# Kernel optimization log

Measured on AMD Instinct MI355X. Metric: run time of the kernel, lower is better.

Reference implementation:

```python
import jax, jax.numpy as jnp
import numpy as np

B, T, HIDDEN = 1, 2048, 2048
N_HEADS, N_KV_HEADS, HEAD_DIM = 32, 8, 64
N_KV_GROUPS = N_HEADS // N_KV_HEADS
MAX_POS = 8192


def _rope_tables(seq_len, head_dim, dtype):
    inv_freq = 1.0 / (10000.0 ** (jnp.arange(0, head_dim, 2, dtype=jnp.float32) / head_dim))
    t = jnp.arange(seq_len, dtype=jnp.float32)
    freqs = jnp.einsum('i,j->ij', t, inv_freq)          # [T, head_dim//2]
    emb = jnp.concatenate([freqs, freqs], axis=-1)      # [T, head_dim]
    cos = jnp.cos(emb)[None, None].astype(dtype)        # [1,1,T,head_dim]
    sin = jnp.sin(emb)[None, None].astype(dtype)
    return cos, sin


def _apply_rotary(x, cos, sin):
    # faithful to original: interleaved rotate-half with cat(freqs,freqs) tables
    x1, x2 = x[..., ::2], x[..., 1::2]
    x_rot = jnp.stack([-x2, x1], axis=-1).reshape(x.shape)
    return x * cos + x_rot * sin


def setup_inputs() -> dict:
    key = jax.random.key(0)
    kx, kq, kk, kv, ko = jax.random.split(key, 5)
    s = 0.02
    return {
        'x':  jax.random.normal(kx, (B, T, HIDDEN), dtype=jnp.float32),
        'Wq': s * jax.random.normal(kq, (N_HEADS * HEAD_DIM, HIDDEN), dtype=jnp.float32),
        'Wk': s * jax.random.normal(kk, (N_KV_HEADS * HEAD_DIM, HIDDEN), dtype=jnp.float32),
        'Wv': s * jax.random.normal(kv, (N_KV_HEADS * HEAD_DIM, HIDDEN), dtype=jnp.float32),
        'Wo': s * jax.random.normal(ko, (HIDDEN, HIDDEN), dtype=jnp.float32),
    }


def reference(x, Wq, Wk, Wv, Wo):
    Bv, Tv, _ = x.shape
    dtype = x.dtype
    # projections (torch Linear: y = x @ W.T), reshape to [B, heads, T, head_dim]
    q = jnp.einsum('bth,oh->bto', x, Wq).reshape(Bv, Tv, N_HEADS, HEAD_DIM).transpose(0, 2, 1, 3)
    k = jnp.einsum('bth,oh->bto', x, Wk).reshape(Bv, Tv, N_KV_HEADS, HEAD_DIM).transpose(0, 2, 1, 3)
    v = jnp.einsum('bth,oh->bto', x, Wv).reshape(Bv, Tv, N_KV_HEADS, HEAD_DIM).transpose(0, 2, 1, 3)
    cos, sin = _rope_tables(Tv, HEAD_DIM, dtype)
    q = _apply_rotary(q, cos, sin)
    k = _apply_rotary(k, cos, sin)
    if N_KV_GROUPS != 1:
        k = jnp.repeat(k, N_KV_GROUPS, axis=1)   # [B, n_heads, T, d]
        v = jnp.repeat(v, N_KV_GROUPS, axis=1)
    scale = 1.0 / jnp.sqrt(jnp.asarray(HEAD_DIM, dtype=dtype))
    scores = jnp.einsum('bhtd,bhsd->bhts', q, k) * scale   # [B,H,T,T]
    causal = jnp.tril(jnp.ones((Tv, Tv), dtype=bool))
    scores = jnp.where(causal[None, None], scores, jnp.asarray(-jnp.inf, dtype=dtype))
    attn = jax.nn.softmax(scores, axis=-1)
    out = jnp.einsum('bhts,bhsd->bhtd', attn, v)
    out = out.transpose(0, 2, 1, 3).reshape(Bv, Tv, HIDDEN)
    return jnp.einsum('bth,oh->bto', out, Wo)
```

## Files before the change

### kernel.cpp

```cpp
#include <hip/hip_runtime.h>
#include <hip/hip_bf16.h>
#include <stdint.h>

#define TT 2048
#define HID 2048
#define NH 32
#define NKV 8
#define HD 64

typedef __attribute__((ext_vector_type(4))) float f32x4;
typedef __attribute__((ext_vector_type(16))) float f32x16;
typedef __attribute__((ext_vector_type(8))) short bf16x8;

__device__ __forceinline__ unsigned short f2bf(float f) {
  unsigned int u = __builtin_bit_cast(unsigned int, f);
  unsigned int r = (u + 0x7FFFu + ((u >> 16) & 1u)) >> 16;
  return (unsigned short)r;
}
__device__ __forceinline__ float bf2f(unsigned short h) {
  unsigned int u = ((unsigned int)h) << 16;
  return __builtin_bit_cast(float, u);
}
__device__ __forceinline__ unsigned int cvtpk(float lo, float hi) {
  unsigned int d;
  asm("v_cvt_pk_bf16_f32 %0, %1, %2" : "=v"(d) : "v"(lo), "v"(hi));
  return d;
}
__device__ __forceinline__ float max3f(float a, float b, float c) {
  float d;
  asm("v_max3_f32 %0, %1, %2, %3" : "=v"(d) : "v"(a), "v"(b), "v"(c));
  return d;
}

__device__ __forceinline__ void gld_lds16(const void* g, void* l) {
  __builtin_amdgcn_global_load_lds(
      (const __attribute__((address_space(1))) unsigned int*)g,
      (__attribute__((address_space(3))) unsigned int*)l,
      16, 0, 0);
}

__global__ __launch_bounds__(256)
void k_cvt_all(const float* __restrict__ x, const float* __restrict__ wq,
               const float* __restrict__ wk, const float* __restrict__ wv,
               const float* __restrict__ wo,
               unsigned short* __restrict__ xb, unsigned short* __restrict__ wqb,
               unsigned short* __restrict__ wkb, unsigned short* __restrict__ wvb,
               unsigned short* __restrict__ wob) {
  int i = blockIdx.x * 256 + threadIdx.x;
  const float* src; unsigned short* dst; int off;
  if      (i < 1048576) { src = x;  dst = xb;  off = i; }
  else if (i < 2097152) { src = wq; dst = wqb; off = i - 1048576; }
  else if (i < 2359296) { src = wk; dst = wkb; off = i - 2097152; }
  else if (i < 2621440) { src = wv; dst = wvb; off = i - 2359296; }
  else if (i < 3670016) { src = wo; dst = wob; off = i - 2621440; }
  else return;
  const float4 v = reinterpret_cast<const float4*>(src)[off];
  ushort4 o;
  o.x = f2bf(v.x); o.y = f2bf(v.y); o.z = f2bf(v.z); o.w = f2bf(v.w);
  reinterpret_cast<ushort4*>(dst)[off] = o;
}

__device__ __forceinline__ void stage_tile(const unsigned short* __restrict__ g,
                                           unsigned short* lds, int w, int l, int k0) {
#pragma unroll
  for (int j = 0; j < 2; ++j) {
    const int cbase = w * 128 + j * 64;
    const int c = cbase + l;
    const int row = c >> 2, off = c & 3;
    gld_lds16(g + row * 2048 + k0 + off * 8, lds + cbase * 8);
  }
}

__device__ __forceinline__ void gemm_core(const unsigned short* __restrict__ A,
                                          const unsigned short* __restrict__ B,
                                          unsigned short* As, unsigned short* Bs,
                                          f32x4 (&acc)[4][4], int kiters) {
  const int tid = threadIdx.x;
  const int l = tid & 63, w = tid >> 6;
  const int wm = w >> 1, wn = w & 1;
  const int ll = l & 15, lg = l >> 4;

  stage_tile(A, As, w, l, 0);
  stage_tile(B, Bs, w, l, 0);
  int cur = 0;
  for (int kt = 0; kt < kiters; ++kt) {
    __syncthreads();
    if (kt + 1 < kiters) {
      stage_tile(A, As + (cur ^ 1) * 4096, w, l, (kt + 1) * 32);
      stage_tile(B, Bs + (cur ^ 1) * 4096, w, l, (kt + 1) * 32);
    }
    const unsigned short* a0 = As + cur * 4096;
    const unsigned short* b0 = Bs + cur * 4096;
    bf16x8 af[4], bfr[4];
#pragma unroll
    for (int i = 0; i < 4; ++i) {
      af[i]  = *reinterpret_cast<const bf16x8*>(a0 + (wm * 64 + i * 16 + ll) * 32 + lg * 8);
      bfr[i] = *reinterpret_cast<const bf16x8*>(b0 + (wn * 64 + i * 16 + ll) * 32 + lg * 8);
    }
#pragma unroll
    for (int i = 0; i < 4; ++i)
#pragma unroll
      for (int j = 0; j < 4; ++j)
        acc[i][j] = __builtin_amdgcn_mfma_f32_16x16x32_bf16(af[i], bfr[j], acc[i][j], 0, 0, 0);
    cur ^= 1;
  }
}

__global__ __launch_bounds__(256)
void k_gemm_qkv(const unsigned short* __restrict__ xb,
                const unsigned short* __restrict__ wq,
                const unsigned short* __restrict__ wk,
                const unsigned short* __restrict__ wv,
                unsigned short* __restrict__ Pq,
                unsigned short* __restrict__ Pk,
                unsigned short* __restrict__ Pv) {
  __shared__ __align__(16) unsigned short As[2 * 4096];
  __shared__ __align__(16) unsigned short Bs[2 * 4096];
  const int bid = blockIdx.x;
  const unsigned short *A, *B;
  int m0, n0, seg, ks;
  if (bid < 640) {
    ks = bid & 1;
    int pair = bid >> 1;
    int mt = pair / 20, nt = pair % 20;
    m0 = mt * 128;
    A = xb + (size_t)m0 * 2048 + ks * 1024;
    if (nt < 16) { seg = 0; n0 = nt * 128; B = wq + (size_t)n0 * 2048 + ks * 1024; }
    else         { seg = 1; n0 = (nt - 16) * 128; B = wk + (size_t)n0 * 2048 + ks * 1024; }
  } else {
    int vb = bid - 640;
    ks = vb & 1;
    int pair = vb >> 1;
    int mt = pair / 16, nt = pair % 16;
    seg = 2; m0 = mt * 128; n0 = nt * 128;
    A = wv + (size_t)m0 * 2048 + ks * 1024;
    B = xb + (size_t)n0 * 2048 + ks * 1024;
  }
  f32x4 acc[4][4] = {};
  gemm_core(A, B, As, Bs, acc, 32);

  const int l = threadIdx.x & 63, w = threadIdx.x >> 6;
  const int wm = w >> 1, wn = w & 1;
#pragma unroll
  for (int i = 0; i < 4; ++i)
#pragma unroll
    for (int j = 0; j < 4; ++j)
#pragma unroll
      for (int r = 0; r < 4; ++r) {
        int row = m0 + wm * 64 + i * 16 + ((l >> 4) << 2) + r;
        int col = n0 + wn * 64 + j * 16 + (l & 15);
        unsigned short v = f2bf(acc[i][j][r]);
        if (seg == 0)      Pq[(size_t)ks * 4194304 + (size_t)row * 2048 + col] = v;
        else if (seg == 1) Pk[(size_t)ks * 1048576 + (size_t)row * 512 + col] = v;
        else               Pv[(size_t)ks * 1048576 + (size_t)row * 2048 + col] = v;
      }
}

__global__ __launch_bounds__(256)
void k_gemm_out(const unsigned short* __restrict__ Ob,
                const unsigned short* __restrict__ wo,
                float* __restrict__ out,
                float* __restrict__ p1a, float* __restrict__ p1b) {
  __shared__ __align__(16) unsigned short As[2 * 4096];
  __shared__ __align__(16) unsigned short Bs[2 * 4096];
  const int bid = blockIdx.x;
  const int ks = bid >> 8;
  const int rem = bid & 255;
  const int m0 = (rem >> 4) * 128, n0 = (rem & 15) * 128;
  f32x4 acc[4][4] = {};
  gemm_core(Ob + (size_t)m0 * 2048 + ks * 1024,
            wo + (size_t)n0 * 2048 + ks * 1024, As, Bs, acc, 32);

  const int l = threadIdx.x & 63, w = threadIdx.x >> 6;
  const int wm = w >> 1, wn = w & 1;
#pragma unroll
  for (int i = 0; i < 4; ++i)
#pragma unroll
    for (int j = 0; j < 4; ++j)
#pragma unroll
      for (int r = 0; r < 4; ++r) {
        int row = m0 + wm * 64 + i * 16 + ((l >> 4) << 2) + r;
        int col = n0 + wn * 64 + j * 16 + (l & 15);
        if (ks == 0) {
          out[(size_t)row * HID + col] = acc[i][j][r];
        } else {
          float* p = (row < 1024) ? (p1a + (size_t)row * HID)
                                  : (p1b + (size_t)(row - 1024) * HID);
          p[col] = acc[i][j][r];
        }
      }
}

__global__ __launch_bounds__(256)
void k_reduce_out(float* __restrict__ out,
                  const float* __restrict__ p1a, const float* __restrict__ p1b) {
  const int i = blockIdx.x * 256 + threadIdx.x;
  const int row = i >> 9;
  const float* p1 = (row < 1024) ? p1a : (p1b - (size_t)1024 * HID);
  const float4 a = reinterpret_cast<const float4*>(out)[i];
  const float4 b = reinterpret_cast<const float4*>(p1)[i];
  float4 c;
  c.x = a.x + b.x; c.y = a.y + b.y; c.z = a.z + b.z; c.w = a.w + b.w;
  reinterpret_cast<float4*>(out)[i] = c;
}

__global__ __launch_bounds__(256)
void k_rope_tab(float2* __restrict__ tab) {
  const int i = blockIdx.x * 256 + threadIdx.x;
  const int t = i >> 6, k = i & 63;
  const float cexp = -13.287712379549449f / 32.0f;
  const float fr = exp2f((float)(k & 31) * cexp);
  const float a = (float)t * fr;
  tab[i] = make_float2(__cosf(a), __sinf(a));
}

__global__ __launch_bounds__(256)
void k_rope_kv(const unsigned short* __restrict__ Pk,
               const unsigned short* __restrict__ Pv,
               const float2* __restrict__ tab,
               unsigned short* __restrict__ Kb,
               unsigned short* __restrict__ VT) {
  int p = blockIdx.x * 256 + threadIdx.x;
  if (p < 524288) {
    const int t = p >> 8;
    const int col2 = (p & 255) * 2;
    const int kh = col2 >> 6, d = col2 & 63;
    const unsigned int u0 = *reinterpret_cast<const unsigned int*>(Pk + (size_t)t * 512 + col2);
    const unsigned int u1 = *reinterpret_cast<const unsigned int*>(Pk + 1048576 + (size_t)t * 512 + col2);
    float x0 = bf2f((unsigned short)(u0 & 0xFFFFu)) + bf2f((unsigned short)(u1 & 0xFFFFu));
    float x1 = bf2f((unsigned short)(u0 >> 16)) + bf2f((unsigned short)(u1 >> 16));
    const float4 cs = *reinterpret_cast<const float4*>(tab + t * 64 + d);
    float o0 = x0 * cs.x - x1 * cs.y;
    float o1 = x1 * cs.z + x0 * cs.w;
    unsigned int pw = (unsigned int)f2bf(o0) | ((unsigned int)f2bf(o1) << 16);
    *reinterpret_cast<unsigned int*>(Kb + ((size_t)kh * 2048 + t) * 64 + d) = pw;
  } else {
    const int i2 = (p - 524288) * 2;
    const unsigned int u0 = *reinterpret_cast<const unsigned int*>(Pv + i2);
    const unsigned int u1 = *reinterpret_cast<const unsigned int*>(Pv + 1048576 + i2);
    float x0 = bf2f((unsigned short)(u0 & 0xFFFFu)) + bf2f((unsigned short)(u1 & 0xFFFFu));
    float x1 = bf2f((unsigned short)(u0 >> 16)) + bf2f((unsigned short)(u1 >> 16));
    unsigned int pw = (unsigned int)f2bf(x0) | ((unsigned int)f2bf(x1) << 16);
    *reinterpret_cast<unsigned int*>(VT + i2) = pw;
  }
}

__global__ __launch_bounds__(256)
void k_rope_q(const unsigned short* __restrict__ Pq,
              const float2* __restrict__ tab,
              unsigned short* __restrict__ Qb) {
  const int p = blockIdx.x * 256 + threadIdx.x;
  const int t = p >> 10;
  const int col2 = (p & 1023) * 2;
  const int h = col2 >> 6, d = col2 & 63;
  const unsigned int u0 = *reinterpret_cast<const unsigned int*>(Pq + (size_t)t * 2048 + col2);
  const unsigned int u1 = *reinterpret_cast<const unsigned int*>(Pq + 4194304 + (size_t)t * 2048 + col2);
  float x0 = bf2f((unsigned short)(u0 & 0xFFFFu)) + bf2f((unsigned short)(u1 & 0xFFFFu));
  float x1 = bf2f((unsigned short)(u0 >> 16)) + bf2f((unsigned short)(u1 >> 16));
  const float scale = 0.125f * 1.4426950408889634f;
  const float4 cs = *reinterpret_cast<const float4*>(tab + t * 64 + d);
  float o0 = (x0 * cs.x - x1 * cs.y) * scale;
  float o1 = (x1 * cs.z + x0 * cs.w) * scale;
  unsigned int pw = (unsigned int)f2bf(o0) | ((unsigned int)f2bf(o1) << 16);
  *reinterpret_cast<unsigned int*>(Qb + ((size_t)h * 2048 + t) * 64 + d) = pw;
}

__device__ __forceinline__ void attn_stage(const unsigned short* __restrict__ Kg,
                                           const unsigned short* __restrict__ Vg,
                                           unsigned short* Ks, unsigned short* Vs,
                                           int kv0, int w, int l) {
#pragma unroll
  for (int j = 0; j < 4; ++j) {
    const int cb = j * 128 + w * 64;
    const int c = cb + l;
    const int row = c >> 3;
    const int src8 = ((c & 7) ^ (row & 7)) * 8;
    gld_lds16(Kg + (size_t)(kv0 + row) * 64 + src8, Ks + cb * 8);
    gld_lds16(Vg + (size_t)row * TT + kv0 + src8, Vs + cb * 8);
  }
}

__global__ __launch_bounds__(128, 2)
void k_attn(const unsigned short* __restrict__ Qb,
            const unsigned short* __restrict__ Kb,
            const unsigned short* __restrict__ VT,
            unsigned short* __restrict__ Ob) {
  __shared__ __align__(16) unsigned short Ks[2][64 * 64];
  __shared__ __align__(16) unsigned short Vs[2][64 * 64];
  const int b = blockIdx.x;
  const int h = b & 31;
  const int qi = b >> 5;
  const int q0 = qi & 7, kq = qi >> 3;
  const int qt = (kq == 0) ? 2 * q0 : (kq == 1) ? 31 - 2 * q0
               : (kq == 2) ? 2 * q0 + 1 : 30 - 2 * q0;
  const int kh = h >> 2;
  const int tid = threadIdx.x;
  const int l = tid & 63, w = tid >> 6;
  const int q = l & 31, hi = l >> 5;
  const int qrow = qt * 64 + w * 32 + q;

  const unsigned short* Qh = Qb + (size_t)h * TT * 64;
  const unsigned short* Kh = Kb + (size_t)kh * TT * 64;
  const unsigned short* Vh = VT + (size_t)kh * 64 * TT;

  bf16x8 qf[4];
#pragma unroll
  for (int s = 0; s < 4; ++s)
    qf[s] = *reinterpret_cast<const bf16x8*>(Qh + (size_t)qrow * 64 + s * 16 + hi * 8);

  f32x16 ot0, ot1;
#pragma unroll
  for (int r = 0; r < 16; ++r) { ot0[r] = 0.f; ot1[r] = 0.f; }
  float m = -3e38f, lsum = 0.f;
  const int nkt = qt + 1;

  attn_stage(Kh, Vh, Ks[0], Vs[0], 0, w, l);
  int cur = 0;
  for (int kt = 0; kt < nkt; ++kt) {
    __syncthreads();
    if (kt + 1 < nkt)
      attn_stage(Kh, Vh, Ks[cur ^ 1], Vs[cur ^ 1], (kt + 1) * 64, w, l);

    const char* Kc = reinterpret_cast<const char*>(Ks[cur]);
    const char* Vc = reinterpret_cast<const char*>(Vs[cur]);

    f32x16 s0, s1;
#pragma unroll
    for (int r = 0; r < 16; ++r) { s0[r] = 0.f; s1[r] = 0.f; }
    __builtin_amdgcn_s_setprio(1);
#pragma unroll
    for (int s = 0; s < 4; ++s) {
      const int chunk = 2 * s + hi;
      const bf16x8 kf0 = *reinterpret_cast<const bf16x8*>(
          Kc + q * 128 + ((chunk ^ (q & 7)) * 16));
      const bf16x8 kf1 = *reinterpret_cast<const bf16x8*>(
          Kc + (32 + q) * 128 + ((chunk ^ (q & 7)) * 16));
      s0 = __builtin_amdgcn_mfma_f32_32x32x16_bf16(kf0, qf[s], s0, 0, 0, 0);
      s1 = __builtin_amdgcn_mfma_f32_32x32x16_bf16(kf1, qf[s], s1, 0, 0, 0);
    }
    __builtin_amdgcn_s_setprio(0);
    if (kt == qt) {
#pragma unroll
      for (int r = 0; r < 16; ++r) {
        const int kvr = kt * 64 + (r & 3) + 8 * (r >> 2) + 4 * hi;
        if (kvr > qrow) s0[r] = -3e38f;
        if (kvr + 32 > qrow) s1[r] = -3e38f;
      }
    }
    float a0 = max3f(s0[0], s0[1], s0[2]);
    float a1 = max3f(s0[3], s0[4], s0[5]);
    float a2 = max3f(s0[6], s0[7], s0[8]);
    float a3 = max3f(s0[9], s0[10], s0[11]);
    float a4 = max3f(s0[12], s0[13], s0[14]);
    float a5 = max3f(s0[15], s1[0], s1[1]);
    float a6 = max3f(s1[2], s1[3], s1[4]);
    float a7 = max3f(s1[5], s1[6], s1[7]);
    float a8 = max3f(s1[8], s1[9], s1[10]);
    float a9 = max3f(s1[11], s1[12], s1[13]);
    float a10 = fmaxf(s1[14], s1[15]);
    float b0 = max3f(a0, a1, a2);
    float b1 = max3f(a3, a4, a5);
    float b2 = max3f(a6, a7, a8);
    float b3 = fmaxf(a9, a10);
    float mloc = fmaxf(max3f(b0, b1, b2), b3);
    mloc = fmaxf(mloc, __shfl_xor(mloc, 32));

    if (!__all(mloc <= m + 8.f)) {
      const float mn = fmaxf(m, mloc);
      const float al = __builtin_amdgcn_exp2f(m - mn);
      m = mn;
      lsum *= al;
#pragma unroll
      for (int r = 0; r < 16; ++r) { ot0[r] *= al; ot1[r] *= al; }
    }
#pragma unroll
    for (int r = 0; r < 16; ++r) {
      s0[r] = __builtin_amdgcn_exp2f(s0[r] - m);
      s1[r] = __builtin_amdgcn_exp2f(s1[r] - m);
    }
    float t16[16];
#pragma unroll
    for (int r = 0; r < 16; ++r) t16[r] = s0[r] + s1[r];
#pragma unroll
    for (int r = 0; r < 8; ++r) t16[r] += t16[r + 8];
#pragma unroll
    for (int r = 0; r < 4; ++r) t16[r] += t16[r + 4];
    float ssum = (t16[0] + t16[1]) + (t16[2] + t16[3]);
    ssum += __shfl_xor(ssum, 32);
    lsum += ssum;

#pragma unroll
    for (int s = 0; s < 4; ++s) {
      const int base = (s & 1) * 8;
      const f32x16& sg = (s < 2) ? s0 : s1;
      const unsigned int c0 = cvtpk(sg[base + 0], sg[base + 1]);
      const unsigned int c1 = cvtpk(sg[base + 2], sg[base + 3]);
      const unsigned int c2 = cvtpk(sg[base + 4], sg[base + 5]);
      const unsigned int c3 = cvtpk(sg[base + 6], sg[base + 7]);
      const unsigned int slo = hi ? c0 : c2, shi_ = hi ? c1 : c3;
      const unsigned int rlo = (unsigned int)__shfl_xor((int)slo, 32);
      const unsigned int rhi = (unsigned int)__shfl_xor((int)shi_, 32);
      union { unsigned int u[4]; bf16x8 v; } P;
      P.u[0] = hi ? rlo : c0;
      P.u[1] = hi ? rhi : c1;
      P.u[2] = hi ? c2 : rlo;
      P.u[3] = hi ? c3 : rhi;
      const int chunk = 2 * s + hi;
      const bf16x8 vf0 = *reinterpret_cast<const bf16x8*>(
          Vc + q * 128 + ((chunk ^ (q & 7)) * 16));
      const bf16x8 vf1 = *reinterpret_cast<const bf16x8*>(
          Vc + (32 + q) * 128 + ((chunk ^ (q & 7)) * 16));
      __builtin_amdgcn_s_setprio(1);
      ot0 = __builtin_amdgcn_mfma_f32_32x32x16_bf16(vf0, P.v, ot0, 0, 0, 0);
      ot1 = __builtin_amdgcn_mfma_f32_32x32x16_bf16(vf1, P.v, ot1, 0, 0, 0);
      __builtin_amdgcn_s_setprio(0);
    }
    cur ^= 1;
  }

  __syncthreads();
  float* Of = reinterpret_cast<float*>(&Ks[0][0]) + w * (64 * 33);
  const float inv = 1.0f / lsum;
#pragma unroll
  for (int r = 0; r < 16; ++r) {
    const int d = (r & 3) + 8 * (r >> 2) + 4 * hi;
    Of[d * 33 + q] = ot0[r] * inv;
    Of[(d + 32) * 33 + q] = ot1[r] * inv;
  }
  __syncthreads();
#pragma unroll
  for (int i = 0; i < 4; ++i) {
    const int a = 4 * hi + i;
    float v[8];
#pragma unroll
    for (int k2 = 0; k2 < 8; ++k2) v[k2] = Of[(a * 8 + k2) * 33 + q];
    union { unsigned int u[4]; uint4 vec; } O4;
    O4.u[0] = cvtpk(v[0], v[1]);
    O4.u[1] = cvtpk(v[2], v[3]);
    O4.u[2] = cvtpk(v[4], v[5]);
    O4.u[3] = cvtpk(v[6], v[7]);
    *reinterpret_cast<uint4*>(Ob + (size_t)qrow * HID + h * 64 + a * 8) = O4.vec;
  }
}

extern "C" void kernel_launch(void* const* d_in, const int* in_sizes, int n_in,
                              void* d_out, int out_size, void* d_ws, size_t ws_size,
                              hipStream_t stream) {
  const float* x  = (const float*)d_in[0];
  const float* Wq = (const float*)d_in[1];
  const float* Wk = (const float*)d_in[2];
  const float* Wv = (const float*)d_in[3];
  const float* Wo = (const float*)d_in[4];
  float* out = (float*)d_out;
  char* ws = (char*)d_ws;

  unsigned short* xb  = (unsigned short*)(ws);
  unsigned short* wqb = (unsigned short*)(ws + (8u  << 20));
  unsigned short* wkb = (unsigned short*)(ws + (16u << 20));
  unsigned short* wvb = (unsigned short*)(ws + (18u << 20));
  unsigned short* wob = (unsigned short*)(ws + (20u << 20));
  unsigned short* Qb  = (unsigned short*)(ws + (28u << 20));
  unsigned short* Kb  = (unsigned short*)(ws + (36u << 20));
  unsigned short* VT  = (unsigned short*)(ws + (38u << 20));
  unsigned short* Ob  = xb;
  float2* tab = (float2*)(ws + (8u << 20));
  unsigned short* Pq = (unsigned short*)d_out;
  unsigned short* Pk = (unsigned short*)(ws + (28u << 20));
  unsigned short* Pv = (unsigned short*)(ws + (32u << 20));
  float* p1a = (float*)(ws + (8u << 20));
  float* p1b = (float*)(ws + (28u << 20));

  k_cvt_all<<<14336, 256, 0, stream>>>(x, Wq, Wk, Wv, Wo, xb, wqb, wkb, wvb, wob);
  k_gemm_qkv<<<768, 256, 0, stream>>>(xb, wqb, wkb, wvb, Pq, Pk, Pv);
  k_rope_tab<<<512, 256, 0, stream>>>(tab);
  k_rope_kv<<<4096, 256, 0, stream>>>(Pk, Pv, tab, Kb, VT);
  k_rope_q<<<8192, 256, 0, stream>>>(Pq, tab, Qb);
  k_attn<<<dim3(1024), 128, 0, stream>>>(Qb, Kb, VT, Ob);
  k_gemm_out<<<512, 256, 0, stream>>>(Ob, wob, out, p1a, p1b);
  k_reduce_out<<<4096, 256, 0, stream>>>(out, p1a, p1b);
}
```

Baseline: 163.3 us.

## Split long causal query tiles across two blocks and merge partial softmax results

```diff
diff --git a/kernel.cpp b/kernel.cpp
--- a/kernel.cpp
+++ b/kernel.cpp
@@ -271,12 +271,11 @@
                                            int kv0, int w, int l) {
 #pragma unroll
   for (int j = 0; j < 4; ++j) {
-    const int cb = j * 128 + w * 64;
-    const int c = cb + l;
-    const int row = c >> 3;
-    const int src8 = ((c & 7) ^ (row & 7)) * 8;
-    gld_lds16(Kg + (size_t)(kv0 + row) * 64 + src8, Ks + cb * 8);
-    gld_lds16(Vg + (size_t)row * TT + kv0 + src8, Vs + cb * 8);
+    const int c = j * 2 + w;
+    unsigned short* kd = Ks + c * 512;
+    unsigned short* vd = Vs + c * 512;
+    gld_lds16(Kg + (size_t)(kv0 + l) * 64 + c * 8, kd);
+    gld_lds16(Vg + (size_t)l * TT + kv0 + c * 8, vd);
   }
 }
 
@@ -284,15 +283,20 @@
 void k_attn(const unsigned short* __restrict__ Qb,
             const unsigned short* __restrict__ Kb,
             const unsigned short* __restrict__ VT,
-            unsigned short* __restrict__ Ob) {
+            unsigned short* __restrict__ Ob,
+            float* __restrict__ PA, float* __restrict__ PB,
+            float* __restrict__ MLb) {
   __shared__ __align__(16) unsigned short Ks[2][64 * 64];
   __shared__ __align__(16) unsigned short Vs[2][64 * 64];
   const int b = blockIdx.x;
   const int h = b & 31;
-  const int qi = b >> 5;
-  const int q0 = qi & 7, kq = qi >> 3;
-  const int qt = (kq == 0) ? 2 * q0 : (kq == 1) ? 31 - 2 * q0
-               : (kq == 2) ? 2 * q0 + 1 : 30 - 2 * q0;
+  const int u = b >> 5;
+  int qt, kt0, kt1, mode;
+  if (u < 16)      { qt = 16 + u; kt0 = 0;  kt1 = 15; mode = 1; }
+  else if (u < 24) { qt = 47 - u; kt0 = 16; kt1 = qt; mode = 2; }
+  else if (u < 32) { qt = u - 8;  kt0 = 16; kt1 = qt; mode = 2; }
+  else if (u < 40) { qt = 47 - u; kt0 = 0;  kt1 = qt; mode = 0; }
+  else             { qt = u - 40; kt0 = 0;  kt1 = qt; mode = 0; }
   const int kh = h >> 2;
   const int tid = threadIdx.x;
   const int l = tid & 63, w = tid >> 6;
@@ -312,17 +316,16 @@
 #pragma unroll
   for (int r = 0; r < 16; ++r) { ot0[r] = 0.f; ot1[r] = 0.f; }
   float m = -3e38f, lsum = 0.f;
-  const int nkt = qt + 1;
-
-  attn_stage(Kh, Vh, Ks[0], Vs[0], 0, w, l);
+
+  attn_stage(Kh, Vh, Ks[0], Vs[0], kt0 * 64, w, l);
   int cur = 0;
-  for (int kt = 0; kt < nkt; ++kt) {
+  for (int kt = kt0; kt <= kt1; ++kt) {
     __syncthreads();
-    if (kt + 1 < nkt)
+    if (kt + 1 <= kt1)
       attn_stage(Kh, Vh, Ks[cur ^ 1], Vs[cur ^ 1], (kt + 1) * 64, w, l);
 
-    const char* Kc = reinterpret_cast<const char*>(Ks[cur]);
-    const char* Vc = reinterpret_cast<const char*>(Vs[cur]);
+    const unsigned short* Kc = Ks[cur];
+    const unsigned short* Vc = Vs[cur];
 
     f32x16 s0, s1;
 #pragma unroll
@@ -330,11 +333,9 @@
     __builtin_amdgcn_s_setprio(1);
 #pragma unroll
     for (int s = 0; s < 4; ++s) {
-      const int chunk = 2 * s + hi;
-      const bf16x8 kf0 = *reinterpret_cast<const bf16x8*>(
-          Kc + q * 128 + ((chunk ^ (q & 7)) * 16));
-      const bf16x8 kf1 = *reinterpret_cast<const bf16x8*>(
-          Kc + (32 + q) * 128 + ((chunk ^ (q & 7)) * 16));
+      const int c = 2 * s + hi;
+      const bf16x8 kf0 = *reinterpret_cast<const bf16x8*>(Kc + (c * 64 + q) * 8);
+      const bf16x8 kf1 = *reinterpret_cast<const bf16x8*>(Kc + (c * 64 + 32 + q) * 8);
       s0 = __builtin_amdgcn_mfma_f32_32x32x16_bf16(kf0, qf[s], s0, 0, 0, 0);
       s1 = __builtin_amdgcn_mfma_f32_32x32x16_bf16(kf1, qf[s], s1, 0, 0, 0);
     }
@@ -405,11 +406,9 @@
       P.u[1] = hi ? rhi : c1;
       P.u[2] = hi ? c2 : rlo;
       P.u[3] = hi ? c3 : rhi;
-      const int chunk = 2 * s + hi;
-      const bf16x8 vf0 = *reinterpret_cast<const bf16x8*>(
-          Vc + q * 128 + ((chunk ^ (q & 7)) * 16));
-      const bf16x8 vf1 = *reinterpret_cast<const bf16x8*>(
-          Vc + (32 + q) * 128 + ((chunk ^ (q & 7)) * 16));
+      const int c = 2 * s + hi;
+      const bf16x8 vf0 = *reinterpret_cast<const bf16x8*>(Vc + (c * 64 + q) * 8);
+      const bf16x8 vf1 = *reinterpret_cast<const bf16x8*>(Vc + (c * 64 + 32 + q) * 8);
       __builtin_amdgcn_s_setprio(1);
       ot0 = __builtin_amdgcn_mfma_f32_32x32x16_bf16(vf0, P.v, ot0, 0, 0, 0);
       ot1 = __builtin_amdgcn_mfma_f32_32x32x16_bf16(vf1, P.v, ot1, 0, 0, 0);
@@ -418,6 +417,20 @@
     cur ^= 1;
   }
 
+  if (mode) {
+    const int pid = (qt - 16) * 32 + h;
+    float* P = (mode == 1 ? PA : PB) + (size_t)pid * 4096 + w * 2048;
+#pragma unroll
+    for (int r = 0; r < 16; ++r) {
+      P[r * 64 + l] = ot0[r];
+      P[(16 + r) * 64 + l] = ot1[r];
+    }
+    const int mlidx = (mode == 1) ? pid : 512 + pid;
+    MLb[(size_t)mlidx * 256 + w * 64 + l] = m;
+    MLb[(size_t)mlidx * 256 + 128 + w * 64 + l] = lsum;
+    return;
+  }
+
   __syncthreads();
   float* Of = reinterpret_cast<float*>(&Ks[0][0]) + w * (64 * 33);
   const float inv = 1.0f / lsum;
@@ -434,6 +447,49 @@
     float v[8];
 #pragma unroll
     for (int k2 = 0; k2 < 8; ++k2) v[k2] = Of[(a * 8 + k2) * 33 + q];
+    union { unsigned int u[4]; uint4 vec; } O4;
+    O4.u[0] = cvtpk(v[0], v[1]);
+    O4.u[1] = cvtpk(v[2], v[3]);
+    O4.u[2] = cvtpk(v[4], v[5]);
+    O4.u[3] = cvtpk(v[6], v[7]);
+    *reinterpret_cast<uint4*>(Ob + (size_t)qrow * HID + h * 64 + a * 8) = O4.vec;
+  }
+}
+
+__global__ __launch_bounds__(128)
+void k_attn_merge(const float* __restrict__ PA, const float* __restrict__ PB,
+                  const float* __restrict__ MLb, unsigned short* __restrict__ Ob) {
+  __shared__ float Of[2 * 64 * 33];
+  const int pid = blockIdx.x;
+  const int h = pid & 31, qt = 16 + (pid >> 5);
+  const int tid = threadIdx.x, l = tid & 63, w = tid >> 6;
+  const int q = l & 31, hi = l >> 5;
+  const float mA = MLb[(size_t)pid * 256 + w * 64 + l];
+  const float lA = MLb[(size_t)pid * 256 + 128 + w * 64 + l];
+  const float mB = MLb[(size_t)(512 + pid) * 256 + w * 64 + l];
+  const float lB = MLb[(size_t)(512 + pid) * 256 + 128 + w * 64 + l];
+  const float M = fmaxf(mA, mB);
+  const float wA = __builtin_amdgcn_exp2f(mA - M);
+  const float wB = __builtin_amdgcn_exp2f(mB - M);
+  const float inv = 1.0f / (lA * wA + lB * wB);
+  const float fA = wA * inv, fB = wB * inv;
+  const float* Pa = PA + (size_t)pid * 4096 + w * 2048;
+  const float* Pb = PB + (size_t)pid * 4096 + w * 2048;
+  float* of = Of + w * (64 * 33);
+#pragma unroll
+  for (int r = 0; r < 16; ++r) {
+    const int d = (r & 3) + 8 * (r >> 2) + 4 * hi;
+    of[d * 33 + q]        = Pa[r * 64 + l] * fA + Pb[r * 64 + l] * fB;
+    of[(d + 32) * 33 + q] = Pa[(16 + r) * 64 + l] * fA + Pb[(16 + r) * 64 + l] * fB;
+  }
+  __syncthreads();
+  const int qrow = qt * 64 + w * 32 + q;
+#pragma unroll
+  for (int i = 0; i < 4; ++i) {
+    const int a = 4 * hi + i;
+    float v[8];
+#pragma unroll
+    for (int k2 = 0; k2 < 8; ++k2) v[k2] = of[(a * 8 + k2) * 33 + q];
     union { unsigned int u[4]; uint4 vec; } O4;
     O4.u[0] = cvtpk(v[0], v[1]);
     O4.u[1] = cvtpk(v[2], v[3]);
@@ -464,9 +520,12 @@
   unsigned short* VT  = (unsigned short*)(ws + (38u << 20));
   unsigned short* Ob  = xb;
   float2* tab = (float2*)(ws + (8u << 20));
+  float* ML   = (float*)(ws + (9u << 20));
   unsigned short* Pq = (unsigned short*)d_out;
   unsigned short* Pk = (unsigned short*)(ws + (28u << 20));
   unsigned short* Pv = (unsigned short*)(ws + (32u << 20));
+  float* PA = (float*)d_out;
+  float* PB = PA + 512 * 4096;
   float* p1a = (float*)(ws + (8u << 20));
   float* p1b = (float*)(ws + (28u << 20));
 
@@ -475,7 +534,8 @@
   k_rope_tab<<<512, 256, 0, stream>>>(tab);
   k_rope_kv<<<4096, 256, 0, stream>>>(Pk, Pv, tab, Kb, VT);
   k_rope_q<<<8192, 256, 0, stream>>>(Pq, tab, Qb);
-  k_attn<<<dim3(1024), 128, 0, stream>>>(Qb, Kb, VT, Ob);
+  k_attn<<<1536, 128, 0, stream>>>(Qb, Kb, VT, Ob, PA, PB, ML);
+  k_attn_merge<<<512, 128, 0, stream>>>(PA, PB, ML, Ob);
   k_gemm_out<<<512, 256, 0, stream>>>(Ob, wob, out, p1a, p1b);
   k_reduce_out<<<4096, 256, 0, stream>>>(out, p1a, p1b);
 }
```

Measured after the change: 169.1 us. 1.04x slower.
